# Kernel tuning notes

Measured on AMD Instinct MI355X. Metric: run time of the kernel, lower is better.

The kernel has to match this reference:

```python
import jax, jax.numpy as jnp
import numpy as np

B, L, D_MODEL = 4, 2048, 2048
N_HEADS, HEAD_DIM = 16, 128
EPS = 1e-6


def _make_rope(key_unused, L, dim, base=10000.0):
    inv_freq = 1.0 / (base ** (np.arange(0, dim, 2, dtype=np.float32) / dim))  # [dim/2]
    t = np.arange(L, dtype=np.float32)
    freqs = np.outer(t, inv_freq)  # [L, dim/2]
    emb = np.concatenate([freqs, freqs], axis=-1)  # [L, dim]
    cos = np.broadcast_to(np.cos(emb)[None], (B, L, dim)).copy()
    sin = np.broadcast_to(np.sin(emb)[None], (B, L, dim)).copy()
    return jnp.asarray(cos), jnp.asarray(sin)


def setup_inputs() -> dict:
    key = jax.random.key(0)
    ks = jax.random.split(key, 8)
    s = 1.0 / np.sqrt(D_MODEL)
    x = jax.random.normal(ks[0], (B, L, D_MODEL), dtype=jnp.float32)
    cos_q, sin_q = _make_rope(None, L, HEAD_DIM)
    cos_k, sin_k = _make_rope(None, L, HEAD_DIM)
    Wq = jax.random.normal(ks[1], (D_MODEL, D_MODEL), dtype=jnp.float32) * s
    Wk = jax.random.normal(ks[2], (D_MODEL, D_MODEL), dtype=jnp.float32) * s
    Wv = jax.random.normal(ks[3], (D_MODEL, D_MODEL), dtype=jnp.float32) * s
    Wo = jax.random.normal(ks[4], (D_MODEL, D_MODEL), dtype=jnp.float32) * s
    q_gamma = jnp.ones((HEAD_DIM,), dtype=jnp.float32) + 0.02 * jax.random.normal(ks[5], (HEAD_DIM,), dtype=jnp.float32)
    k_gamma = jnp.ones((HEAD_DIM,), dtype=jnp.float32) + 0.02 * jax.random.normal(ks[6], (HEAD_DIM,), dtype=jnp.float32)
    return dict(x=x, cos_q=cos_q, sin_q=sin_q, cos_k=cos_k, sin_k=sin_k,
                Wq=Wq, Wk=Wk, Wv=Wv, Wo=Wo, q_gamma=q_gamma, k_gamma=k_gamma)


def _rms_norm(h, w):
    # T5-style RMSNorm over last dim (head_dim), variance in fp32
    var = jnp.mean(h.astype(jnp.float32) ** 2, axis=-1, keepdims=True)
    return w * (h * jax.lax.rsqrt(var + EPS))


def _rotate_half(x):
    d = x.shape[-1] // 2
    return jnp.concatenate([-x[..., d:], x[..., :d]], axis=-1)


def _apply_rope(x, cos, sin):
    # x: [B, L, H, Dh]; cos/sin: [B, L, Dh] -> broadcast over heads
    c = cos[:, :, None, :]
    s = sin[:, :, None, :]
    return x * c + _rotate_half(x) * s


def reference(x, cos_q, sin_q, cos_k, sin_k, Wq, Wk, Wv, Wo, q_gamma, k_gamma):
    Bx, Lx, _ = x.shape
    # QKV projections (Linear with weight [out, in]: y = x @ W.T)
    q = (x @ Wq.T).reshape(Bx, Lx, N_HEADS, HEAD_DIM)
    k = (x @ Wk.T).reshape(Bx, Lx, N_HEADS, HEAD_DIM)
    v = (x @ Wv.T).reshape(Bx, Lx, N_HEADS, HEAD_DIM)
    # per-head QK RMSNorm
    q = _rms_norm(q, q_gamma)
    k = _rms_norm(k, k_gamma)
    # dual RoPE
    q = _apply_rope(q, cos_q, sin_q)
    k = _apply_rope(k, cos_k, sin_k)
    # scaled dot-product attention (dense, no mask)
    scale = 1.0 / jnp.sqrt(jnp.asarray(HEAD_DIM, dtype=x.dtype))
    scores = jnp.einsum('blhd,bmhd->bhlm', q, k) * scale
    attn = jax.nn.softmax(scores, axis=-1)
    out = jnp.einsum('bhlm,bmhd->blhd', attn, v)
    out = out.reshape(Bx, Lx, N_HEADS * HEAD_DIM)
    return out @ Wo.T
```

## Files before the change

### kernel.cpp

```cpp
#include <hip/hip_runtime.h>
#include <stdint.h>

#define DM   2048
#define LSEQ 2048
#define NB   4
#define NH   16
#define HD   128
#define BL   (NB*LSEQ)
#define NK64 (DM/32)

typedef unsigned short u16;
typedef short  short8  __attribute__((ext_vector_type(8)));
typedef short  short4v __attribute__((ext_vector_type(4)));
typedef float  f32x4   __attribute__((ext_vector_type(4)));
typedef float  f32x16  __attribute__((ext_vector_type(16)));

#define LOG2E 1.4426950408889634f

__device__ __forceinline__ float bf2f(u16 v) {
    union { unsigned u; float f; } x; x.u = ((unsigned)v) << 16; return x.f;
}
__device__ __forceinline__ u16 f2bf(float f) {
    union { float f; unsigned u; } x; x.f = f;
    return (u16)((x.u + 0x7FFF + ((x.u >> 16) & 1)) >> 16);
}

#define BAR_LGKM() do {                                        \
    asm volatile("s_waitcnt lgkmcnt(0)" ::: "memory");         \
    __builtin_amdgcn_sched_barrier(0);                         \
    __builtin_amdgcn_s_barrier();                              \
    __builtin_amdgcn_sched_barrier(0);                         \
} while (0)

__device__ __forceinline__ short8 ld8(const void* base, size_t e, bool f32) {
    if (f32) {
        const float* p = (const float*)base + e;
        f32x4 a = *(const f32x4*)p;
        f32x4 b = *(const f32x4*)(p + 4);
        short8 r;
        #pragma unroll
        for (int i = 0; i < 4; ++i) { r[i] = (short)f2bf(a[i]); r[4+i] = (short)f2bf(b[i]); }
        return r;
    }
    return *(const short8*)((const u16*)base + e);
}
__device__ __forceinline__ float lde(const void* b, size_t e, bool f32) {
    return f32 ? ((const float*)b)[e] : bf2f(((const u16*)b)[e]);
}
__device__ __forceinline__ void st1(void* b, size_t e, float v, bool f32) {
    if (f32) ((float*)b)[e] = v; else ((u16*)b)[e] = f2bf(v);
}

extern "C" __global__ void dtype_probe(const u16* __restrict__ x, int* __restrict__ cnt) {
    int t = threadIdx.x;
    int insane = 0;
    #pragma unroll
    for (int j = 0; j < 16; ++j) {
        u16 u = x[t * 16 + j];
        int e = (u >> 7) & 0xFF;
        if (u != 0 && (e < 96 || e > 143)) insane++;
    }
    atomicAdd(cnt, insane);
}

extern "C" __global__ void to_bf16(const void* __restrict__ in, u16* __restrict__ out,
                                   int n8, const int* __restrict__ cnt)
{
    const bool isf = *cnt > 100;
    int i = blockIdx.x * 256 + threadIdx.x;
    if (i >= n8) return;
    *(short8*)(out + (size_t)i * 8) = ld8(in, (size_t)i * 8, isf);
}

extern "C" __global__ void to_bf16_w(const void* w0, const void* w1,
                                     const void* w2, const void* w3,
                                     u16* o0, u16* o1, u16* o2, u16* o3,
                                     int n8, const int* __restrict__ cnt)
{
    const bool isf = *cnt > 100;
    int i = blockIdx.x * 256 + threadIdx.x;
    if (i >= n8) return;
    const void* in; u16* out;
    switch (blockIdx.y) {
        case 0:  in = w0; out = o0; break;
        case 1:  in = w1; out = o1; break;
        case 2:  in = w2; out = o2; break;
        default: in = w3; out = o3; break;
    }
    *(short8*)(out + (size_t)i * 8) = ld8(in, (size_t)i * 8, isf);
}

__device__ __forceinline__ int swz128(int row, int col) {
    return row*128 + ((((col >> 3) ^ row) & 15) << 3) + (col & 7);
}
__device__ __forceinline__ int swz64(int row, int col) {
    return row*64 + ((((col >> 3) ^ row) & 7) << 3) + (col & 7);
}

__device__ __forceinline__ void xcd_swz8(int& bx, int& by, int& bz) {
    const int lin = blockIdx.x + (blockIdx.y << 3) + (blockIdx.z << 8);
    const int nq  = (gridDim.z << 8) >> 3;
    const int nid = (lin & 7) * nq + (lin >> 3);
    bx = nid & 7; by = (nid >> 3) & 31; bz = nid >> 8;
}

typedef __attribute__((address_space(1))) const unsigned int guint;
typedef __attribute__((address_space(3))) unsigned int luint;
__device__ __forceinline__ void gl_lds16(const void* g, void* l) {
    __builtin_amdgcn_global_load_lds((guint*)g, (luint*)l, 16, 0, 0);
}

__device__ __forceinline__ void g256_stage(const u16* ag, const u16* wg,
                                           u16* buf, int k0, int wofs)
{
    gl_lds16(ag + k0,                    buf + wofs);
    gl_lds16(ag + k0 + (size_t)128 * DM, buf + 4096 + wofs);
    gl_lds16(wg + k0,                    buf + 8192 + wofs);
    gl_lds16(wg + k0 + (size_t)128 * DM, buf + 12288 + wofs);
}

__device__ __forceinline__ void g256_core(const u16* __restrict__ A,
                                          const u16* __restrict__ W,
                                          u16* lds, f32x4 acc[8][4],
                                          int m0, int n0, int t)
{
    const int lane = t & 63, w = t >> 6;
    const int quad = lane >> 4, l15 = lane & 15;
    const int wr = (w >> 2) * 128, wc = (w & 3) * 64;
    const int srow = t >> 2;
    const int scol = ((((t & 3) - (t >> 3)) & 3) << 3);
    const u16* ag = A + (size_t)(m0 + srow) * DM + scol;
    const u16* wg = W + (size_t)(n0 + srow) * DM + scol;
    const int wofs = w * 512;
    const int rq = (((quad + (l15 >> 1)) & 3) << 3);

    #pragma unroll
    for (int i = 0; i < 8; ++i)
        #pragma unroll
        for (int j = 0; j < 4; ++j) acc[i][j] = (f32x4){0.f, 0.f, 0.f, 0.f};

    g256_stage(ag, wg, lds,          0, wofs);
    g256_stage(ag, wg, lds + 16384, 32, wofs);
    g256_stage(ag, wg, lds + 32768, 64, wofs);
    asm volatile("s_waitcnt vmcnt(8)" ::: "memory");
    __builtin_amdgcn_sched_barrier(0);
    __builtin_amdgcn_s_barrier();
    __builtin_amdgcn_sched_barrier(0);

    for (int kt = 0; kt < NK64; ++kt) {
        if (kt + 3 < NK64)
            g256_stage(ag, wg, lds + ((kt + 3) & 3) * 16384, (kt + 3) * 32, wofs);
        const u16* Ab = lds + (kt & 3) * 16384;
        const u16* Bb = Ab + 8192;
        short8 afr[8], bfr[4];
        #pragma unroll
        for (int nt = 0; nt < 4; ++nt)
            bfr[nt] = *(const short8*)&Bb[(wc + nt*16 + l15)*32 + rq];
        #pragma unroll
        for (int mt = 0; mt < 8; ++mt)
            afr[mt] = *(const short8*)&Ab[(wr + mt*16 + l15)*32 + rq];
        __builtin_amdgcn_s_setprio(1);
        #pragma unroll
        for (int mt = 0; mt < 8; ++mt)
            #pragma unroll
            for (int nt = 0; nt < 4; ++nt)
                acc[mt][nt] = __builtin_amdgcn_mfma_f32_16x16x32_bf16(
                                  afr[mt], bfr[nt], acc[mt][nt], 0, 0, 0);
        __builtin_amdgcn_s_setprio(0);
        if      (kt <  NK64 - 3) asm volatile("s_waitcnt vmcnt(8)" ::: "memory");
        else if (kt == NK64 - 3) asm volatile("s_waitcnt vmcnt(4)" ::: "memory");
        else if (kt == NK64 - 2) asm volatile("s_waitcnt vmcnt(0)" ::: "memory");
        if (kt < NK64 - 1) {
            __builtin_amdgcn_sched_barrier(0);
            __builtin_amdgcn_s_barrier();
            __builtin_amdgcn_sched_barrier(0);
        }
    }
}

extern "C" __global__ __launch_bounds__(512, 1) void gemm256_bf(
    const u16* __restrict__ A, const u16* __restrict__ W,
    void* __restrict__ O, const int* __restrict__ cnt, int o_sel)
{
    __shared__ __align__(16) u16 lds[65536];
    const bool of = o_sel && (*cnt > 100);
    int bx, by, bz;  xcd_swz8(bx, by, bz);
    const int n0 = bx * 256, m0 = by * 256;
    const int t = threadIdx.x, lane = t & 63;
    const int quad = lane >> 4, l15 = lane & 15;
    const int wr = ((t >> 6) >> 2) * 128, wc = ((t >> 6) & 3) * 64;

    f32x4 acc[8][4];
    g256_core(A, W, lds, acc, m0, n0, t);

    #pragma unroll
    for (int mt = 0; mt < 8; ++mt)
        #pragma unroll
        for (int r = 0; r < 4; ++r) {
            size_t base = (size_t)(m0 + wr + mt*16 + quad*4 + r) * DM + n0 + wc + l15;
            #pragma unroll
            for (int nt = 0; nt < 4; ++nt) st1(O, base + nt*16, acc[mt][nt][r], of);
        }
}

extern "C" __global__ __launch_bounds__(512, 1) void gemm256_proj(
    const u16* __restrict__ A,
    const u16* __restrict__ Wq, const u16* __restrict__ Wk, const u16* __restrict__ Wv,
    u16* __restrict__ Oq, u16* __restrict__ Ok, u16* __restrict__ vT)
{
    __shared__ __align__(16) u16 lds[65536];
    int bx, by, bz;  xcd_swz8(bx, by, bz);
    const u16* W = (bz == 0) ? Wv : (bz == 1 ? Wq : Wk);
    const int n0 = bx * 256, m0 = by * 256;
    const int t = threadIdx.x, lane = t & 63;
    const int quad = lane >> 4, l15 = lane & 15;
    const int wr = ((t >> 6) >> 2) * 128, wc = ((t >> 6) & 3) * 64;

    f32x4 acc[8][4];
    g256_core(A, W, lds, acc, m0, n0, t);

    if (bz == 0) {
        const int b  = m0 >> 11;
        const int l0 = (m0 & (LSEQ - 1)) + wr + quad*4;
        #pragma unroll
        for (int mt = 0; mt < 8; ++mt)
            #pragma unroll
            for (int nt = 0; nt < 4; ++nt) {
                short4v sv;
                #pragma unroll
                for (int r = 0; r < 4; ++r) sv[r] = (short)f2bf(acc[mt][nt][r]);
                int n = n0 + wc + nt*16 + l15;
                *(short4v*)(vT + (size_t)b*DM*LSEQ + (size_t)n*LSEQ + l0 + mt*16) = sv;
            }
    } else {
        u16* O = (bz == 1) ? Oq : Ok;
        #pragma unroll
        for (int mt = 0; mt < 8; ++mt)
            #pragma unroll
            for (int r = 0; r < 4; ++r) {
                size_t base = (size_t)(m0 + wr + mt*16 + quad*4 + r) * DM + n0 + wc + l15;
                #pragma unroll
                for (int nt = 0; nt < 4; ++nt) O[base + nt*16] = f2bf(acc[mt][nt][r]);
            }
    }
}

extern "C" __global__ void rmsrope(u16* __restrict__ q, u16* __restrict__ kk,
    const void* cq, const void* sq, const void* ck, const void* sk,
    const void* qg, const void* kg, const int* cnt)
{
    const bool isf = *cnt > 100;
    const float slc = 0.08838834764831845f * LOG2E;
    int t = blockIdx.x * 256 + threadIdx.x;
    int lane = t & 63;
    int widx = t >> 6;
    int h  = widx & (NH - 1);
    int bl = widx >> 4;
    size_t ro = (size_t)bl * DM + (size_t)h * HD;
    size_t co = (size_t)bl * HD;

    {
        float e0 = bf2f(q[ro + lane]), e1 = bf2f(q[ro + lane + 64]);
        float ss = e0*e0 + e1*e1;
        #pragma unroll
        for (int sm = 1; sm < 64; sm <<= 1) ss += __shfl_xor(ss, sm, 64);
        float r = rsqrtf(ss * (1.f / HD) + 1e-6f);
        float y0 = e0 * r * lde(qg, lane, isf);
        float y1 = e1 * r * lde(qg, lane + 64, isf);
        float c0 = lde(cq, co + lane, isf), c1 = lde(cq, co + lane + 64, isf);
        float s0 = lde(sq, co + lane, isf), s1 = lde(sq, co + lane + 64, isf);
        q[ro + lane]      = f2bf((y0 * c0 - y1 * s0) * slc);
        q[ro + lane + 64] = f2bf((y1 * c1 + y0 * s1) * slc);
    }
    {
        float e0 = bf2f(kk[ro + lane]), e1 = bf2f(kk[ro + lane + 64]);
        float ss = e0*e0 + e1*e1;
        #pragma unroll
        for (int sm = 1; sm < 64; sm <<= 1) ss += __shfl_xor(ss, sm, 64);
        float r = rsqrtf(ss * (1.f / HD) + 1e-6f);
        float y0 = e0 * r * lde(kg, lane, isf);
        float y1 = e1 * r * lde(kg, lane + 64, isf);
        float c0 = lde(ck, co + lane, isf), c1 = lde(ck, co + lane + 64, isf);
        float s0 = lde(sk, co + lane, isf), s1 = lde(sk, co + lane + 64, isf);
        kk[ro + lane]      = f2bf(y0 * c0 - y1 * s0);
        kk[ro + lane + 64] = f2bf(y1 * c1 + y0 * s1);
    }
}

extern "C" __global__ __launch_bounds__(256, 2) void flash(
    const u16* q, const u16* __restrict__ k,
    const u16* __restrict__ vT, u16* o)
{
    __shared__ __align__(16) u16 lds[32768];

    const int bh = blockIdx.x, b = bh >> 4, h = bh & 15;
    const int q0 = blockIdx.y * 128;
    const int t = threadIdx.x, lane = t & 63, w = t >> 6;
    const int l31 = lane & 31, hi8 = (lane >> 5) * 8;
    const size_t qko = (size_t)b * LSEQ * DM + (size_t)h * HD;
    const size_t vo  = (size_t)b * DM * LSEQ + (size_t)h * HD * LSEQ;

    short8 qf[8];
    #pragma unroll
    for (int ks = 0; ks < 8; ++ks)
        qf[ks] = *(const short8*)(q + qko +
                  (size_t)(q0 + w*32 + l31) * DM + ks*16 + hi8);

    f32x16 zz;
    #pragma unroll
    for (int r = 0; r < 16; ++r) zz[r] = 0.f;
    f32x16 acc[4];
    f32x16 dacc;
    #pragma unroll
    for (int dt = 0; dt < 4; ++dt) acc[dt] = zz;
    dacc = zz;

    const short onev = (l31 == 0) ? (short)0x3F80 : (short)0;
    const short8 onesA = {onev, onev, onev, onev, onev, onev, onev, onev};

    const int krow = t >> 4,  kc8 = (t & 15) * 8;
    const int vrow = t >> 3,  vc8 = (t & 7) * 8;
    short8 kreg[4], vreg[4];

    #pragma unroll
    for (int it = 0; it < 4; ++it) {
        kreg[it] = *(const short8*)(k  + qko + (size_t)(krow + it*16) * DM + kc8);
        vreg[it] = *(const short8*)(vT + vo  + (size_t)(vrow + it*32) * LSEQ + vc8);
    }
    {
        u16* Kn = lds;  u16* Vn = lds + 8192;
        #pragma unroll
        for (int it = 0; it < 4; ++it) {
            *(short8*)&Kn[swz128(krow + it*16, kc8)] = kreg[it];
            *(short8*)&Vn[swz64 (vrow + it*32, vc8)] = vreg[it];
        }
    }
    #pragma unroll
    for (int it = 0; it < 4; ++it) {
        kreg[it] = *(const short8*)(k  + qko + (size_t)(64 + krow + it*16) * DM + kc8);
        vreg[it] = *(const short8*)(vT + vo  + (size_t)(vrow + it*32) * LSEQ + 64 + vc8);
    }
    __syncthreads();

    const int NT = LSEQ / 64;
    for (int it0 = 0; it0 < NT; ++it0) {
        const int cur = it0 & 1;
        if (it0 + 1 < NT) {
            asm volatile("s_waitcnt vmcnt(0)" ::: "memory");
            __builtin_amdgcn_sched_barrier(0);
            u16* Kn = lds + (cur ^ 1) * 16384;
            u16* Vn = Kn + 8192;
            #pragma unroll
            for (int it = 0; it < 4; ++it) {
                *(short8*)&Kn[swz128(krow + it*16, kc8)] = kreg[it];
                *(short8*)&Vn[swz64 (vrow + it*32, vc8)] = vreg[it];
            }
        }
        if (it0 + 2 < NT) {
            const int kv = (it0 + 2) * 64;
            #pragma unroll
            for (int it = 0; it < 4; ++it) {
                kreg[it] = *(const short8*)(k  + qko + (size_t)(kv + krow + it*16) * DM + kc8);
                vreg[it] = *(const short8*)(vT + vo  + (size_t)(vrow + it*32) * LSEQ + kv + vc8);
            }
        }
        u16* Kl = lds + cur * 16384;
        u16* Vl = Kl + 8192;

        f32x16 S0, S1;
        __builtin_amdgcn_s_setprio(1);
        {
            short8 kf0 = *(const short8*)&Kl[swz128(l31,      hi8)];
            short8 kf1 = *(const short8*)&Kl[swz128(32 + l31, hi8)];
            S0 = __builtin_amdgcn_mfma_f32_32x32x16_bf16(kf0, qf[0], zz, 0, 0, 0);
            S1 = __builtin_amdgcn_mfma_f32_32x32x16_bf16(kf1, qf[0], zz, 0, 0, 0);
        }
        #pragma unroll
        for (int ks = 1; ks < 8; ++ks) {
            short8 kf0 = *(const short8*)&Kl[swz128(l31,      ks*16 + hi8)];
            short8 kf1 = *(const short8*)&Kl[swz128(32 + l31, ks*16 + hi8)];
            S0 = __builtin_amdgcn_mfma_f32_32x32x16_bf16(kf0, qf[ks], S0, 0, 0, 0);
            S1 = __builtin_amdgcn_mfma_f32_32x32x16_bf16(kf1, qf[ks], S1, 0, 0, 0);
        }
        __builtin_amdgcn_s_setprio(0);

        float p[32];
        #pragma unroll
        for (int r = 0; r < 16; ++r) p[r]      = exp2f(S0[r]);
        #pragma unroll
        for (int r = 0; r < 16; ++r) p[16 + r] = exp2f(S1[r]);

        #pragma unroll
        for (int kt = 0; kt < 2; ++kt) {
            unsigned pk[8];
            #pragma unroll
            for (int j = 0; j < 8; ++j)
                asm("v_cvt_pk_bf16_f32 %0, %1, %2"
                    : "=v"(pk[j]) : "v"(p[kt*16 + 2*j]), "v"(p[kt*16 + 2*j + 1]));
            asm volatile("v_permlane32_swap_b32 %0, %1" : "+v"(pk[0]), "+v"(pk[2]));
            asm volatile("v_permlane32_swap_b32 %0, %1" : "+v"(pk[1]), "+v"(pk[3]));
            asm volatile("v_permlane32_swap_b32 %0, %1" : "+v"(pk[4]), "+v"(pk[6]));
            asm volatile("v_permlane32_swap_b32 %0, %1" : "+v"(pk[5]), "+v"(pk[7]));
            union { unsigned u[4]; short8 v; } f0, f1;
            f0.u[0] = pk[0]; f0.u[1] = pk[1]; f0.u[2] = pk[2]; f0.u[3] = pk[3];
            f1.u[0] = pk[4]; f1.u[1] = pk[5]; f1.u[2] = pk[6]; f1.u[3] = pk[7];
            #pragma unroll
            for (int s = 0; s < 2; ++s) {
                short8 pf = s ? f1.v : f0.v;
                int slice = kt*2 + s;
                __builtin_amdgcn_s_setprio(1);
                #pragma unroll
                for (int dt = 0; dt < 4; ++dt) {
                    short8 vf = *(const short8*)&Vl[swz64(dt*32 + l31, slice*16 + hi8)];
                    acc[dt] = __builtin_amdgcn_mfma_f32_32x32x16_bf16(vf, pf, acc[dt], 0, 0, 0);
                }
                dacc = __builtin_amdgcn_mfma_f32_32x32x16_bf16(onesA, pf, dacc, 0, 0, 0);
                __builtin_amdgcn_s_setprio(0);
            }
        }
        BAR_LGKM();
    }

    __syncthreads();
    u16* Ol = lds + w * 4352;
    float dn0 = dacc[0];
    float dnx = __shfl_xor(dn0, 32, 64);
    float inv = 1.f / ((lane & 32) ? dnx : dn0);
    #pragma unroll
    for (int dt = 0; dt < 4; ++dt)
        #pragma unroll
        for (int i = 0; i < 8; ++i) {
            float a0 = acc[dt][2*i]     * inv;
            float a1 = acc[dt][2*i + 1] * inv;
            unsigned pkv;
            asm("v_cvt_pk_bf16_f32 %0, %1, %2" : "=v"(pkv) : "v"(a0), "v"(a1));
            int d = dt*32 + ((i & 1) << 1) + ((i >> 1) << 3) + ((lane >> 5) << 2);
            *(unsigned*)&Ol[l31*136 + d] = pkv;
        }
    __syncthreads();
    #pragma unroll
    for (int j = 0; j < 8; ++j) {
        int cb = (lane >> 5) + 2*j;
        short8 vv = *(const short8*)&Ol[l31*136 + cb*8];
        *(short8*)(o + qko + (size_t)(q0 + w*32 + l31) * DM + cb*8) = vv;
    }
}

extern "C" void kernel_launch(void* const* d_in, const int* in_sizes, int n_in,
                              void* d_out, int out_size, void* d_ws, size_t ws_size,
                              hipStream_t stream)
{
    const void* x  = d_in[0];
    const void* cq = d_in[1];
    const void* sq = d_in[2];
    const void* ck = d_in[3];
    const void* sk = d_in[4];
    const void* Wq = d_in[5];
    const void* Wk = d_in[6];
    const void* Wv = d_in[7];
    const void* Wo = d_in[8];
    const void* qg = d_in[9];
    const void* kg = d_in[10];

    u16* qws = (u16*)d_ws;
    u16* kws = qws + (size_t)BL * DM;
    u16* vtw = kws + (size_t)BL * DM;
    u16* wqs = vtw + (size_t)BL * DM;
    u16* wks = wqs + (size_t)DM * DM;
    u16* wvs = wks + (size_t)DM * DM;
    u16* wos = wvs + (size_t)DM * DM;
    int* cnt = (int*)(wos + (size_t)DM * DM);
    u16* xb  = (u16*)d_out;

    const int xn8 = BL * DM / 8;
    const int wn8 = DM * DM / 8;

    hipMemsetAsync(cnt, 0, 4, stream);
    dtype_probe<<<1, 256, 0, stream>>>((const u16*)x, cnt);

    to_bf16<<<xn8 / 256, 256, 0, stream>>>(x, xb, xn8, cnt);
    to_bf16_w<<<dim3(wn8 / 256, 4), 256, 0, stream>>>(Wq, Wk, Wv, Wo,
                                                      wqs, wks, wvs, wos, wn8, cnt);

    gemm256_proj<<<dim3(8, 32, 3), 512, 0, stream>>>(xb, wqs, wks, wvs,
                                                     qws, kws, vtw);

    rmsrope<<<dim3(BL * NH / 4), 256, 0, stream>>>(qws, kws, cq, sq, ck, sk, qg, kg, cnt);

    flash<<<dim3(64, 16), 256, 0, stream>>>(qws, kws, vtw, qws);

    gemm256_bf<<<dim3(8, 32), 512, 0, stream>>>(qws, wos, d_out, cnt, 1);
}
```

Before: 673.6 us.

## Merge dtype conversion kernels, split GEMM k-step into halves, widen flash blocks

Result: slower. 995.8 us (+47.8%).

```diff
diff --git a/kernel.cpp b/kernel.cpp
--- a/kernel.cpp
+++ b/kernel.cpp
@@ -32,6 +32,12 @@
     __builtin_amdgcn_sched_barrier(0);                         \
 } while (0)
 
+#define BAR_RAW() do {                                         \
+    __builtin_amdgcn_sched_barrier(0);                         \
+    __builtin_amdgcn_s_barrier();                              \
+    __builtin_amdgcn_sched_barrier(0);                         \
+} while (0)
+
 __device__ __forceinline__ short8 ld8(const void* base, size_t e, bool f32) {
     if (f32) {
         const float* p = (const float*)base + e;
@@ -63,31 +69,32 @@
     atomicAdd(cnt, insane);
 }
 
-extern "C" __global__ void to_bf16(const void* __restrict__ in, u16* __restrict__ out,
-                                   int n8, const int* __restrict__ cnt)
+extern "C" __global__ void to_bf16_all(const void* __restrict__ x,
+                                       const void* w0, const void* w1,
+                                       const void* w2, const void* w3,
+                                       u16* __restrict__ xo,
+                                       u16* o0, u16* o1, u16* o2, u16* o3,
+                                       int wn8, const int* __restrict__ cnt)
 {
     const bool isf = *cnt > 100;
     int i = blockIdx.x * 256 + threadIdx.x;
-    if (i >= n8) return;
-    *(short8*)(out + (size_t)i * 8) = ld8(in, (size_t)i * 8, isf);
-}
-
-extern "C" __global__ void to_bf16_w(const void* w0, const void* w1,
-                                     const void* w2, const void* w3,
-                                     u16* o0, u16* o1, u16* o2, u16* o3,
-                                     int n8, const int* __restrict__ cnt)
-{
-    const bool isf = *cnt > 100;
-    int i = blockIdx.x * 256 + threadIdx.x;
-    if (i >= n8) return;
-    const void* in; u16* out;
-    switch (blockIdx.y) {
-        case 0:  in = w0; out = o0; break;
-        case 1:  in = w1; out = o1; break;
-        case 2:  in = w2; out = o2; break;
-        default: in = w3; out = o3; break;
-    }
-    *(short8*)(out + (size_t)i * 8) = ld8(in, (size_t)i * 8, isf);
+    if (i >= wn8) return;
+    if (blockIdx.y == 0) {
+        #pragma unroll
+        for (int j = 0; j < 4; ++j) {
+            size_t e = (size_t)(i + j * wn8) * 8;
+            *(short8*)(xo + e) = ld8(x, e, isf);
+        }
+    } else {
+        const void* in; u16* out;
+        switch (blockIdx.y) {
+            case 1:  in = w0; out = o0; break;
+            case 2:  in = w1; out = o1; break;
+            case 3:  in = w2; out = o2; break;
+            default: in = w3; out = o3; break;
+        }
+        *(short8*)(out + (size_t)i * 8) = ld8(in, (size_t)i * 8, isf);
+    }
 }
 
 __device__ __forceinline__ int swz128(int row, int col) {
@@ -143,25 +150,23 @@
     g256_stage(ag, wg, lds + 16384, 32, wofs);
     g256_stage(ag, wg, lds + 32768, 64, wofs);
     asm volatile("s_waitcnt vmcnt(8)" ::: "memory");
-    __builtin_amdgcn_sched_barrier(0);
-    __builtin_amdgcn_s_barrier();
-    __builtin_amdgcn_sched_barrier(0);
+    BAR_RAW();
 
     for (int kt = 0; kt < NK64; ++kt) {
         if (kt + 3 < NK64)
             g256_stage(ag, wg, lds + ((kt + 3) & 3) * 16384, (kt + 3) * 32, wofs);
         const u16* Ab = lds + (kt & 3) * 16384;
         const u16* Bb = Ab + 8192;
-        short8 afr[8], bfr[4];
+        short8 afr[4], bfr[4];
         #pragma unroll
         for (int nt = 0; nt < 4; ++nt)
             bfr[nt] = *(const short8*)&Bb[(wc + nt*16 + l15)*32 + rq];
         #pragma unroll
-        for (int mt = 0; mt < 8; ++mt)
+        for (int mt = 0; mt < 4; ++mt)
             afr[mt] = *(const short8*)&Ab[(wr + mt*16 + l15)*32 + rq];
         __builtin_amdgcn_s_setprio(1);
         #pragma unroll
-        for (int mt = 0; mt < 8; ++mt)
+        for (int mt = 0; mt < 4; ++mt)
             #pragma unroll
             for (int nt = 0; nt < 4; ++nt)
                 acc[mt][nt] = __builtin_amdgcn_mfma_f32_16x16x32_bf16(
@@ -170,11 +175,19 @@
         if      (kt <  NK64 - 3) asm volatile("s_waitcnt vmcnt(8)" ::: "memory");
         else if (kt == NK64 - 3) asm volatile("s_waitcnt vmcnt(4)" ::: "memory");
         else if (kt == NK64 - 2) asm volatile("s_waitcnt vmcnt(0)" ::: "memory");
-        if (kt < NK64 - 1) {
-            __builtin_amdgcn_sched_barrier(0);
-            __builtin_amdgcn_s_barrier();
-            __builtin_amdgcn_sched_barrier(0);
-        }
+        BAR_RAW();
+        #pragma unroll
+        for (int mt = 0; mt < 4; ++mt)
+            afr[mt] = *(const short8*)&Ab[(wr + 64 + mt*16 + l15)*32 + rq];
+        __builtin_amdgcn_s_setprio(1);
+        #pragma unroll
+        for (int mt = 0; mt < 4; ++mt)
+            #pragma unroll
+            for (int nt = 0; nt < 4; ++nt)
+                acc[4 + mt][nt] = __builtin_amdgcn_mfma_f32_16x16x32_bf16(
+                                      afr[mt], bfr[nt], acc[4 + mt][nt], 0, 0, 0);
+        __builtin_amdgcn_s_setprio(0);
+        if (kt < NK64 - 1) BAR_RAW();
     }
 }
 
@@ -287,14 +300,14 @@
     }
 }
 
-extern "C" __global__ __launch_bounds__(256, 2) void flash(
+extern "C" __global__ __launch_bounds__(512, 4) void flash(
     const u16* q, const u16* __restrict__ k,
     const u16* __restrict__ vT, u16* o)
 {
-    __shared__ __align__(16) u16 lds[32768];
+    __shared__ __align__(16) u16 lds[34816];
 
     const int bh = blockIdx.x, b = bh >> 4, h = bh & 15;
-    const int q0 = blockIdx.y * 128;
+    const int q0 = blockIdx.y * 256;
     const int t = threadIdx.x, lane = t & 63, w = t >> 6;
     const int l31 = lane & 31, hi8 = (lane >> 5) * 8;
     const size_t qko = (size_t)b * LSEQ * DM + (size_t)h * HD;
@@ -320,25 +333,25 @@
 
     const int krow = t >> 4,  kc8 = (t & 15) * 8;
     const int vrow = t >> 3,  vc8 = (t & 7) * 8;
-    short8 kreg[4], vreg[4];
-
-    #pragma unroll
-    for (int it = 0; it < 4; ++it) {
-        kreg[it] = *(const short8*)(k  + qko + (size_t)(krow + it*16) * DM + kc8);
-        vreg[it] = *(const short8*)(vT + vo  + (size_t)(vrow + it*32) * LSEQ + vc8);
+    short8 kreg[2], vreg[2];
+
+    #pragma unroll
+    for (int it = 0; it < 2; ++it) {
+        kreg[it] = *(const short8*)(k  + qko + (size_t)(krow + it*32) * DM + kc8);
+        vreg[it] = *(const short8*)(vT + vo  + (size_t)(vrow + it*64) * LSEQ + vc8);
     }
     {
         u16* Kn = lds;  u16* Vn = lds + 8192;
         #pragma unroll
-        for (int it = 0; it < 4; ++it) {
-            *(short8*)&Kn[swz128(krow + it*16, kc8)] = kreg[it];
-            *(short8*)&Vn[swz64 (vrow + it*32, vc8)] = vreg[it];
-        }
-    }
-    #pragma unroll
-    for (int it = 0; it < 4; ++it) {
-        kreg[it] = *(const short8*)(k  + qko + (size_t)(64 + krow + it*16) * DM + kc8);
-        vreg[it] = *(const short8*)(vT + vo  + (size_t)(vrow + it*32) * LSEQ + 64 + vc8);
+        for (int it = 0; it < 2; ++it) {
+            *(short8*)&Kn[swz128(krow + it*32, kc8)] = kreg[it];
+            *(short8*)&Vn[swz64 (vrow + it*64, vc8)] = vreg[it];
+        }
+    }
+    #pragma unroll
+    for (int it = 0; it < 2; ++it) {
+        kreg[it] = *(const short8*)(k  + qko + (size_t)(64 + krow + it*32) * DM + kc8);
+        vreg[it] = *(const short8*)(vT + vo  + (size_t)(vrow + it*64) * LSEQ + 64 + vc8);
     }
     __syncthreads();
 
@@ -351,17 +364,17 @@
             u16* Kn = lds + (cur ^ 1) * 16384;
             u16* Vn = Kn + 8192;
             #pragma unroll
-            for (int it = 0; it < 4; ++it) {
-                *(short8*)&Kn[swz128(krow + it*16, kc8)] = kreg[it];
-                *(short8*)&Vn[swz64 (vrow + it*32, vc8)] = vreg[it];
+            for (int it = 0; it < 2; ++it) {
+                *(short8*)&Kn[swz128(krow + it*32, kc8)] = kreg[it];
+                *(short8*)&Vn[swz64 (vrow + it*64, vc8)] = vreg[it];
             }
         }
         if (it0 + 2 < NT) {
             const int kv = (it0 + 2) * 64;
             #pragma unroll
-            for (int it = 0; it < 4; ++it) {
-                kreg[it] = *(const short8*)(k  + qko + (size_t)(kv + krow + it*16) * DM + kc8);
-                vreg[it] = *(const short8*)(vT + vo  + (size_t)(vrow + it*32) * LSEQ + kv + vc8);
+            for (int it = 0; it < 2; ++it) {
+                kreg[it] = *(const short8*)(k  + qko + (size_t)(kv + krow + it*32) * DM + kc8);
+                vreg[it] = *(const short8*)(vT + vo  + (size_t)(vrow + it*64) * LSEQ + kv + vc8);
             }
         }
         u16* Kl = lds + cur * 16384;
@@ -472,22 +485,20 @@
     int* cnt = (int*)(wos + (size_t)DM * DM);
     u16* xb  = (u16*)d_out;
 
-    const int xn8 = BL * DM / 8;
     const int wn8 = DM * DM / 8;
 
     hipMemsetAsync(cnt, 0, 4, stream);
     dtype_probe<<<1, 256, 0, stream>>>((const u16*)x, cnt);
 
-    to_bf16<<<xn8 / 256, 256, 0, stream>>>(x, xb, xn8, cnt);
-    to_bf16_w<<<dim3(wn8 / 256, 4), 256, 0, stream>>>(Wq, Wk, Wv, Wo,
-                                                      wqs, wks, wvs, wos, wn8, cnt);
+    to_bf16_all<<<dim3(wn8 / 256, 5), 256, 0, stream>>>(
+        x, Wq, Wk, Wv, Wo, xb, wqs, wks, wvs, wos, wn8, cnt);
 
     gemm256_proj<<<dim3(8, 32, 3), 512, 0, stream>>>(xb, wqs, wks, wvs,
                                                      qws, kws, vtw);
 
     rmsrope<<<dim3(BL * NH / 4), 256, 0, stream>>>(qws, kws, cq, sq, ck, sk, qg, kg, cnt);
 
-    flash<<<dim3(64, 16), 256, 0, stream>>>(qws, kws, vtw, qws);
+    flash<<<dim3(64, 8), 512, 0, stream>>>(qws, kws, vtw, qws);
 
     gemm256_bf<<<dim3(8, 32), 512, 0, stream>>>(qws, wos, d_out, cnt, 1);
 }
```
